# Performance work log

Measured on AMD Instinct MI355X. Metric: run time of the kernel, lower is better.

## Reference

```python
import jax, jax.numpy as jnp
import numpy as np

D, H, KVH, HD, FF = 768, 12, 4, 64, 2048
N_REP = H // KVH
EPS = 1e-6


def rmsnorm(x, w):
    # Faithful to source: norm = ||x|| * n^{-1/2}; eps added to norm (not inside sqrt)
    norm = jnp.sqrt(jnp.sum(x * x, axis=-1, keepdims=True)) * (x.shape[-1] ** -0.5)
    return w * x / (norm + EPS)


def rope_tables(seq_len, head_dim, base=10000.0):
    inv_freq = 1.0 / (base ** (np.arange(0, head_dim, 2, dtype=np.float32) / head_dim))
    t = np.arange(seq_len, dtype=np.float32)
    freqs = np.einsum('i,j->ij', t, inv_freq)  # [S, HD/2]
    emb = np.concatenate([freqs, freqs], axis=-1)  # [S, HD]
    return jnp.asarray(np.cos(emb)), jnp.asarray(np.sin(emb))


def rotate_half(x):
    h = x.shape[-1] // 2
    return jnp.concatenate([-x[..., h:], x[..., :h]], axis=-1)


def setup_inputs() -> dict:
    key = jax.random.key(0)
    ks = jax.random.split(key, 9)
    s = 0.02
    return {
        'x': jax.random.normal(ks[0], (2, 2048, D), jnp.float32),
        'Wq': jax.random.normal(ks[1], (H * HD, D), jnp.float32) * s,
        'Wk': jax.random.normal(ks[2], (KVH * HD, D), jnp.float32) * s,
        'Wv': jax.random.normal(ks[3], (KVH * HD, D), jnp.float32) * s,
        'Wo': jax.random.normal(ks[4], (D, H * HD), jnp.float32) * s,
        'Wgate': jax.random.normal(ks[5], (FF, D), jnp.float32) * s,
        'Wup': jax.random.normal(ks[6], (FF, D), jnp.float32) * s,
        'Wdown': jax.random.normal(ks[7], (D, FF), jnp.float32) * s,
        'g1': jnp.ones((D,), jnp.float32),
        'g2': jnp.ones((D,), jnp.float32),
    }


def reference(x, Wq, Wk, Wv, Wo, Wgate, Wup, Wdown, g1, g2):
    B, S, _ = x.shape
    # ---- attention sublayer (pre-norm) ----
    xn = rmsnorm(x, g1)
    q = (xn @ Wq.T).reshape(B, S, H, HD).transpose(0, 2, 1, 3)      # [B,H,S,HD]
    k = (xn @ Wk.T).reshape(B, S, KVH, HD).transpose(0, 2, 1, 3)    # [B,KVH,S,HD]
    v = (xn @ Wv.T).reshape(B, S, KVH, HD).transpose(0, 2, 1, 3)
    cos, sin = rope_tables(S, HD)                                   # [S,HD]
    q = q * cos + rotate_half(q) * sin
    k = k * cos + rotate_half(k) * sin
    # repeat kv heads to match q heads
    k = jnp.repeat(k, N_REP, axis=1)                                # [B,H,S,HD]
    v = jnp.repeat(v, N_REP, axis=1)
    scores = jnp.einsum('bhqd,bhkd->bhqk', q, k) / jnp.sqrt(jnp.float32(HD))
    causal = jnp.tril(jnp.ones((S, S), bool))
    scores = jnp.where(causal, scores, jnp.finfo(scores.dtype).min)
    attn = jax.nn.softmax(scores, axis=-1)
    out = jnp.einsum('bhqk,bhkd->bhqd', attn, v)                    # [B,H,S,HD]
    out = out.transpose(0, 2, 1, 3).reshape(B, S, H * HD) @ Wo.T
    x = x + out
    # ---- SwiGLU FFN sublayer (pre-norm) ----
    xn2 = rmsnorm(x, g2)
    ff = (jax.nn.silu(xn2 @ Wgate.T) * (xn2 @ Wup.T)) @ Wdown.T
    return x + ff
```

## Files before the change

### kernel.cpp

```cpp
#include <hip/hip_runtime.h>
#include <hip/hip_bf16.h>
#include <math.h>

typedef __bf16 bf16;
typedef __attribute__((ext_vector_type(8))) __bf16 bf16x8;
typedef __attribute__((ext_vector_type(4))) __bf16 bf16x4;
typedef __attribute__((ext_vector_type(4))) float f32x4;

#define MFMA16(a,b,c) __builtin_amdgcn_mfma_f32_16x16x32_bf16(a,b,c,0,0,0)

#define BATCH 2
#define SEQ   2048
#define DMODEL 768
#define NH    12
#define NKV   4
#define NREP  3
#define HD    64
#define FFDIM 2048
#define ROWS  (BATCH*SEQ)

#define QSCALE 0.18033688011112042f
#define LOG2E  1.4426950408889634f

#define WB(N) asm volatile("s_waitcnt vmcnt(" #N ")\n\ts_barrier" ::: "memory")
#define BAR() asm volatile("s_barrier" ::: "memory")

__device__ __forceinline__ void gl2lds16(const bf16* g, bf16* l) {
  __builtin_amdgcn_global_load_lds(
      (const __attribute__((address_space(1))) void*)g,
      (__attribute__((address_space(3))) void*)l, 16, 0, 0);
}

struct Cvt7 { const float* s[7]; bf16* d[7]; int n[7]; };
__global__ __launch_bounds__(256) void cvt_all_kernel(Cvt7 c) {
  int seg = blockIdx.y;
  const float* __restrict__ src = c.s[seg];
  bf16* __restrict__ dst = c.d[seg];
  int n = c.n[seg];
  int stride = gridDim.x * 256;
  for (int i = blockIdx.x * 256 + threadIdx.x; i < n; i += stride)
    dst[i] = (bf16)src[i];
}

__global__ __launch_bounds__(256) void rope_tab_kernel(float* __restrict__ tab) {
  int id = blockIdx.x * 256 + threadIdx.x;
  int j = id >> 11, s = id & 2047;
  float inv = expf(-(float)j * (9.210340371976184f / 32.0f));
  float ang = (float)s * inv;
  tab[id] = cosf(ang);
  tab[65536 + id] = sinf(ang);
}

__global__ __launch_bounds__(192) void rmsnorm_kernel(const float* __restrict__ x,
    const float* __restrict__ g, bf16* __restrict__ out) {
  int row = blockIdx.x;
  const float* xr = x + (size_t)row * DMODEL;
  int t = threadIdx.x;
  f32x4 v = *(const f32x4*)(xr + t * 4);
  float ss = v[0] * v[0] + v[1] * v[1] + v[2] * v[2] + v[3] * v[3];
  #pragma unroll
  for (int off = 32; off; off >>= 1) ss += __shfl_xor(ss, off, 64);
  __shared__ float red[3];
  if ((t & 63) == 0) red[t >> 6] = ss;
  __syncthreads();
  float total = red[0] + red[1] + red[2];
  float norm = sqrtf(total) * 0.03608439182435161f;
  float sc = 1.0f / (norm + 1e-6f);
  f32x4 gv = *(const f32x4*)(g + t * 4);
  bf16x4 o;
  #pragma unroll
  for (int i = 0; i < 4; ++i) o[i] = (bf16)(gv[i] * v[i] * sc);
  *(bf16x4*)(out + (size_t)row * DMODEL + t * 4) = o;
}

__global__ __launch_bounds__(512, 6) void gemm_out_kernel(const bf16* __restrict__ A,
    const bf16* __restrict__ B, float* __restrict__ C, const float* __restrict__ R,
    int N, int K) {
  __shared__ __align__(16) bf16 At[2][3][64 * 32];
  __shared__ __align__(16) bf16 Bt[2][3][64 * 32];
  int t = threadIdx.x;
  int g = t >> 8;
  int tt = t & 255;
  int lane = t & 63;
  int w = (t >> 6) & 3;
  int l15 = lane & 15, lq = lane >> 4;
  int wrow = (w >> 1) * 32, wcol = (w & 1) * 32;

  int flat = blockIdx.y * 12 + blockIdx.x;
  int f2 = (flat & 7) * 96 + (flat >> 3);
  int col0 = (f2 % 12) * 64, row0 = (f2 / 12) * 64;

  const int KH = K >> 1;
  const int NS = KH / 32;
  const bf16* Ag = A + (size_t)(row0 + (tt >> 2)) * K + g * KH + (tt & 3) * 8;
  const bf16* Bg = B + (size_t)(col0 + (tt >> 2)) * K + g * KH + (tt & 3) * 8;

  #pragma unroll
  for (int s = 0; s < 3; ++s) {
    gl2lds16(Ag + s * 32, At[g][s] + tt * 8);
    gl2lds16(Bg + s * 32, Bt[g][s] + tt * 8);
  }

  f32x4 zero = {0.f, 0.f, 0.f, 0.f};
  f32x4 acc[2][2];
  #pragma unroll
  for (int m = 0; m < 2; ++m)
    #pragma unroll
    for (int n = 0; n < 2; ++n) acc[m][n] = zero;

  #define OG_COMPUTE(slot) do {                                              \
    const bf16* at = At[g][slot]; const bf16* bt = Bt[g][slot];              \
    bf16x8 af[2], bb[2];                                                     \
    _Pragma("unroll")                                                        \
    for (int m = 0; m < 2; ++m)                                              \
      af[m] = *(const bf16x8*)(at + (wrow + m * 16 + l15) * 32 + lq * 8);    \
    _Pragma("unroll")                                                        \
    for (int n = 0; n < 2; ++n)                                              \
      bb[n] = *(const bf16x8*)(bt + (wcol + n * 16 + l15) * 32 + lq * 8);    \
    _Pragma("unroll")                                                        \
    for (int m = 0; m < 2; ++m)                                              \
      _Pragma("unroll")                                                      \
      for (int n = 0; n < 2; ++n)                                            \
        acc[m][n] = MFMA16(af[m], bb[n], acc[m][n]);                         \
  } while (0)

  int slot = 0;
  for (int k = 0; k < NS - 2; ++k) {
    WB(4);
    OG_COMPUTE(slot);
    BAR();
    if (k <= NS - 4) {
      int ks = (k + 3) * 32;
      gl2lds16(Ag + ks, At[g][slot] + tt * 8);
      gl2lds16(Bg + ks, Bt[g][slot] + tt * 8);
    }
    slot = (slot == 2) ? 0 : slot + 1;
  }
  for (int k = NS - 2; k < NS; ++k) {
    WB(0);
    OG_COMPUTE(slot);
    slot = (slot == 2) ? 0 : slot + 1;
  }
  #undef OG_COMPUTE

  __syncthreads();
  float* Cl = (float*)&At[0][0][0];
  if (g == 1) {
    #pragma unroll
    for (int m = 0; m < 2; ++m)
      #pragma unroll
      for (int n = 0; n < 2; ++n)
        #pragma unroll
        for (int r = 0; r < 4; ++r)
          Cl[(wrow + m * 16 + lq * 4 + r) * 64 + wcol + n * 16 + l15] = acc[m][n][r];
  }
  __syncthreads();
  if (g == 0) {
    #pragma unroll
    for (int m = 0; m < 2; ++m)
      #pragma unroll
      for (int n = 0; n < 2; ++n)
        #pragma unroll
        for (int r = 0; r < 4; ++r) {
          int row = wrow + m * 16 + lq * 4 + r;
          int col = wcol + n * 16 + l15;
          size_t idx = (size_t)(row0 + row) * N + col0 + col;
          C[idx] = acc[m][n][r] + Cl[row * 64 + col] + R[idx];
        }
  }
}

__global__ __launch_bounds__(256) void gemm_qkv_kernel(const bf16* __restrict__ A,
    const bf16* __restrict__ Wcat, const float* __restrict__ tab,
    bf16* __restrict__ Qh, bf16* __restrict__ Kh, bf16* __restrict__ Vt) {
  __shared__ __align__(16) bf16 At[4][64 * 32];
  __shared__ __align__(16) bf16 Bt[4][128 * 32];
  const int K = DMODEL;
  int t = threadIdx.x, lane = t & 63, wave = t >> 6;
  int l15 = lane & 15, lq = lane >> 4;
  int wrow = (wave >> 1) * 32, wcol = (wave & 1) * 64;
  int row0 = blockIdx.y * 64, col0 = blockIdx.x * 128;
  const bf16* Ag  = A + (size_t)(row0 + (t >> 2)) * K + (t & 3) * 8;
  const bf16* Bg0 = Wcat + (size_t)(col0 + (t >> 2)) * K + (t & 3) * 8;
  const bf16* Bg1 = Bg0 + (size_t)64 * K;
  const int NS = K / 32;

  #pragma unroll
  for (int s = 0; s < 4; ++s) {
    int ks = s * 32;
    gl2lds16(Ag + ks,  At[s] + t * 8);
    gl2lds16(Bg0 + ks, Bt[s] + t * 8);
    gl2lds16(Bg1 + ks, Bt[s] + 2048 + t * 8);
  }

  f32x4 zero = {0.f, 0.f, 0.f, 0.f};
  f32x4 acc[2][4];
  #pragma unroll
  for (int m = 0; m < 2; ++m)
    #pragma unroll
    for (int n = 0; n < 4; ++n) acc[m][n] = zero;

  #define QK_COMPUTE(slot) do {                                              \
    const bf16* at = At[slot]; const bf16* bt = Bt[slot];                    \
    bf16x8 af[2], bfr[4];                                                    \
    _Pragma("unroll")                                                        \
    for (int m = 0; m < 2; ++m)                                              \
      af[m] = *(const bf16x8*)(at + (wrow + m * 16 + l15) * 32 + lq * 8);    \
    _Pragma("unroll")                                                        \
    for (int n = 0; n < 4; ++n)                                              \
      bfr[n] = *(const bf16x8*)(bt + (wcol + n * 16 + l15) * 32 + lq * 8);   \
    _Pragma("unroll")                                                        \
    for (int m = 0; m < 2; ++m)                                              \
      _Pragma("unroll")                                                      \
      for (int n = 0; n < 4; ++n)                                            \
        acc[m][n] = MFMA16(af[m], bfr[n], acc[m][n]);                        \
  } while (0)

  for (int k = 0; k < NS - 3; ++k) {
    WB(9);
    QK_COMPUTE(k & 3);
    BAR();
    if (k <= NS - 5) {
      int ks = (k + 4) * 32;
      gl2lds16(Ag + ks,  At[k & 3] + t * 8);
      gl2lds16(Bg0 + ks, Bt[k & 3] + t * 8);
      gl2lds16(Bg1 + ks, Bt[k & 3] + 2048 + t * 8);
    }
  }
  for (int k = NS - 3; k < NS; ++k) {
    WB(0);
    QK_COMPUTE(k & 3);
  }
  #undef QK_COMPUTE

  int b = row0 >> 11;
  int s0 = (row0 & 2047) + wrow + lq * 4;
  int colw = col0 + wcol;
  if (colw < 768) {
    int h = colw >> 6;
    f32x4 cv[2][2], sv[2][2];
    #pragma unroll
    for (int m = 0; m < 2; ++m)
      #pragma unroll
      for (int jh = 0; jh < 2; ++jh) {
        const float* cp = tab + (jh * 16 + l15) * 2048 + s0 + m * 16;
        cv[m][jh] = *(const f32x4*)cp;
        sv[m][jh] = *(const f32x4*)(cp + 65536);
      }
    #pragma unroll
    for (int m = 0; m < 2; ++m)
      #pragma unroll
      for (int n = 0; n < 4; ++n) {
        float sgn = (n < 2) ? -1.f : 1.f;
        #pragma unroll
        for (int r = 0; r < 4; ++r) {
          float c = cv[m][n & 1][r], si = sv[m][n & 1][r];
          float rp = (acc[m][n][r] * c + sgn * acc[m][n ^ 2][r] * si) * QSCALE;
          Qh[((size_t)(b * NH + h) * SEQ + s0 + m * 16 + r) * 64 + n * 16 + l15] = (bf16)rp;
        }
      }
  } else if (colw < 1024) {
    int kh = (colw - 768) >> 6;
    f32x4 cv[2][2], sv[2][2];
    #pragma unroll
    for (int m = 0; m < 2; ++m)
      #pragma unroll
      for (int jh = 0; jh < 2; ++jh) {
        const float* cp = tab + (jh * 16 + l15) * 2048 + s0 + m * 16;
        cv[m][jh] = *(const f32x4*)cp;
        sv[m][jh] = *(const f32x4*)(cp + 65536);
      }
    #pragma unroll
    for (int m = 0; m < 2; ++m)
      #pragma unroll
      for (int n = 0; n < 4; ++n) {
        float sgn = (n < 2) ? -1.f : 1.f;
        #pragma unroll
        for (int r = 0; r < 4; ++r) {
          float c = cv[m][n & 1][r], si = sv[m][n & 1][r];
          float rp = acc[m][n][r] * c + sgn * acc[m][n ^ 2][r] * si;
          Kh[((size_t)(b * NKV + kh) * SEQ + s0 + m * 16 + r) * 64 + n * 16 + l15] = (bf16)rp;
        }
      }
  } else {
    int vh = (colw - 1024) >> 6;
    #pragma unroll
    for (int m = 0; m < 2; ++m)
      #pragma unroll
      for (int n = 0; n < 4; ++n) {
        bf16x4 pv;
        #pragma unroll
        for (int r = 0; r < 4; ++r) pv[r] = (bf16)acc[m][n][r];
        *(bf16x4*)(Vt + ((size_t)(b * NKV + vh) * 64 + n * 16 + l15) * SEQ + s0 + m * 16) = pv;
      }
  }
}

__global__ __launch_bounds__(512, 4) void gemm_gu_kernel(const bf16* __restrict__ A,
    const bf16* __restrict__ Wg, const bf16* __restrict__ Wu, bf16* __restrict__ H) {
  __shared__ __align__(16) bf16 At[3][128 * 32];
  __shared__ __align__(16) bf16 Bgt[3][128 * 32];
  __shared__ __align__(16) bf16 But[3][128 * 32];
  const int K = DMODEL;
  int t = threadIdx.x, lane = t & 63, wave = t >> 6;
  int l15 = lane & 15, lq = lane >> 4;
  int wrow = (wave >> 2) * 64, wcol = (wave & 3) * 32;
  int row0 = blockIdx.y * 128, col0 = blockIdx.x * 128;
  const bf16* Ag = A  + (size_t)(row0 + (t >> 2)) * K + (t & 3) * 8;
  const bf16* Gg = Wg + (size_t)(col0 + (t >> 2)) * K + (t & 3) * 8;
  const bf16* Ug = Wu + (size_t)(col0 + (t >> 2)) * K + (t & 3) * 8;
  const int NS = K / 32;

  #pragma unroll
  for (int s = 0; s < 3; ++s) {
    int ks = s * 32;
    gl2lds16(Ag + ks, At[s] + t * 8);
    gl2lds16(Gg + ks, Bgt[s] + t * 8);
    gl2lds16(Ug + ks, But[s] + t * 8);
  }

  f32x4 zero = {0.f, 0.f, 0.f, 0.f};
  f32x4 ag[4][2], au[4][2];
  #pragma unroll
  for (int m = 0; m < 4; ++m)
    #pragma unroll
    for (int n = 0; n < 2; ++n) { ag[m][n] = zero; au[m][n] = zero; }

  #define GU_COMPUTE(slot) do {                                              \
    const bf16* at = At[slot];                                               \
    const bf16* bgt = Bgt[slot]; const bf16* but = But[slot];                \
    bf16x8 af[4], bg[2], bu[2];                                              \
    _Pragma("unroll")                                                        \
    for (int m = 0; m < 4; ++m)                                              \
      af[m] = *(const bf16x8*)(at + (wrow + m * 16 + l15) * 32 + lq * 8);    \
    _Pragma("unroll")                                                        \
    for (int n = 0; n < 2; ++n) {                                            \
      bg[n] = *(const bf16x8*)(bgt + (wcol + n * 16 + l15) * 32 + lq * 8);   \
      bu[n] = *(const bf16x8*)(but + (wcol + n * 16 + l15) * 32 + lq * 8);   \
    }                                                                        \
    _Pragma("unroll")                                                        \
    for (int m = 0; m < 4; ++m)                                              \
      _Pragma("unroll")                                                      \
      for (int n = 0; n < 2; ++n) {                                          \
        ag[m][n] = MFMA16(af[m], bg[n], ag[m][n]);                           \
        au[m][n] = MFMA16(af[m], bu[n], au[m][n]);                           \
      }                                                                      \
  } while (0)

  int slot = 0;
  for (int k = 0; k < NS - 2; ++k) {
    WB(6);
    GU_COMPUTE(slot);
    BAR();
    if (k <= NS - 4) {
      int ks = (k + 3) * 32;
      gl2lds16(Ag + ks, At[slot] + t * 8);
      gl2lds16(Gg + ks, Bgt[slot] + t * 8);
      gl2lds16(Ug + ks, But[slot] + t * 8);
    }
    slot = (slot == 2) ? 0 : slot + 1;
  }
  for (int k = NS - 2; k < NS; ++k) {
    WB(0);
    GU_COMPUTE(slot);
    slot = (slot == 2) ? 0 : slot + 1;
  }
  #undef GU_COMPUTE

  #pragma unroll
  for (int m = 0; m < 4; ++m)
    #pragma unroll
    for (int n = 0; n < 2; ++n)
      #pragma unroll
      for (int r = 0; r < 4; ++r) {
        int row = row0 + wrow + m * 16 + lq * 4 + r;
        int col = col0 + wcol + n * 16 + l15;
        float g = ag[m][n][r], u = au[m][n][r];
        float sg = g / (1.f + __builtin_amdgcn_exp2f(-g * LOG2E));
        H[(size_t)row * FFDIM + col] = (bf16)(sg * u);
      }
}

__global__ __launch_bounds__(256) void attn_kernel(const bf16* __restrict__ Qh,
    const bf16* __restrict__ Kh, const bf16* __restrict__ Vt, bf16* __restrict__ out) {
  __shared__ __align__(16) bf16 Kl0[2][64 * 32];
  __shared__ __align__(16) bf16 Kl1[2][64 * 32];
  __shared__ __align__(16) bf16 Vl0[2][64 * 32];
  __shared__ __align__(16) bf16 Vl1[2][64 * 32];
  __shared__ __align__(16) bf16 P[4][16 * 80];

  int idx = blockIdx.x;
  int qt = 31 - (idx / 24);
  int bh = idx % 24;
  int q0blk = qt * 64;
  int b = bh / NH, h = bh % NH;
  int kvh = h / NREP;
  int t = threadIdx.x;
  int lane = t & 63, wave = t >> 6;
  int l15 = lane & 15, lq = lane >> 4;
  int qw = q0blk + wave * 16;
  const bf16* Qb = Qh + (size_t)(b * NH + h) * SEQ * 64;
  const bf16* Kb = Kh + (size_t)(b * NKV + kvh) * SEQ * 64;
  const bf16* Vb = Vt + (size_t)(b * NKV + kvh) * 64 * SEQ;

  bf16x8 bq0 = *(const bf16x8*)(Qb + (size_t)(qw + l15) * 64 + lq * 8);
  bf16x8 bq1 = *(const bf16x8*)(Qb + (size_t)(qw + l15) * 64 + 32 + lq * 8);

  const bf16* Kg = Kb + (size_t)(t >> 2) * 64 + (t & 3) * 8;
  const bf16* Vg = Vb + (size_t)(t >> 2) * SEQ + (t & 3) * 8;
  bf16* Pw = P[wave];
  int Pwq = l15 * 80, lq8 = lq * 8, lq4 = lq * 4;
  const int NS = qt + 1;

  #pragma unroll
  for (int s = 0; s < 2; ++s) {
    int ks = (s < NS ? s : NS - 1) * 64;
    gl2lds16(Kg + (size_t)ks * 64,      Kl0[s] + t * 8);
    gl2lds16(Kg + (size_t)ks * 64 + 32, Kl1[s] + t * 8);
    gl2lds16(Vg + ks,                   Vl0[s] + t * 8);
    gl2lds16(Vg + ks + 32,              Vl1[s] + t * 8);
  }

  f32x4 zero = {0.f, 0.f, 0.f, 0.f};
  f32x4 o[4];
  o[0] = zero; o[1] = zero; o[2] = zero; o[3] = zero;
  float l_r = 0.f;

  #define ATTN_STEP(kk, slot) do {                                           \
    int k0 = (kk) * 64;                                                      \
    const bf16* kl0 = Kl0[slot]; const bf16* kl1 = Kl1[slot];                \
    const bf16* vl0 = Vl0[slot]; const bf16* vl1 = Vl1[slot];                \
    f32x4 s[4];                                                              \
    _Pragma("unroll")                                                        \
    for (int c = 0; c < 4; ++c) {                                            \
      bf16x8 ak0 = *(const bf16x8*)(kl0 + (c * 16 + l15) * 32 + lq8);        \
      bf16x8 ak1 = *(const bf16x8*)(kl1 + (c * 16 + l15) * 32 + lq8);        \
      s[c] = zero;                                                           \
      s[c] = MFMA16(ak0, bq0, s[c]);                                         \
      s[c] = MFMA16(ak1, bq1, s[c]);                                         \
    }                                                                        \
    if (k0 + 63 > qw) {                                                      \
      int qmk = qw + l15 - k0 - lq4;                                         \
      _Pragma("unroll")                                                      \
      for (int c = 0; c < 4; ++c)                                            \
        _Pragma("unroll")                                                    \
        for (int r = 0; r < 4; ++r)                                          \
          if (c * 16 + r > qmk) s[c][r] = -INFINITY;                         \
    }                                                                        \
    _Pragma("unroll")                                                        \
    for (int c = 0; c < 4; ++c) {                                            \
      bf16x4 pe;                                                             \
      _Pragma("unroll")                                                      \
      for (int r = 0; r < 4; ++r) {                                          \
        float e = __builtin_amdgcn_exp2f(s[c][r]);                           \
        l_r += e;                                                            \
        pe[r] = (bf16)e;                                                     \
      }                                                                      \
      *(bf16x4*)(Pw + Pwq + c * 16 + lq4) = pe;                              \
    }                                                                        \
    bf16x8 bp0 = *(const bf16x8*)(Pw + Pwq + lq8);                           \
    bf16x8 bp1 = *(const bf16x8*)(Pw + Pwq + 32 + lq8);                      \
    _Pragma("unroll")                                                        \
    for (int n = 0; n < 4; ++n) {                                            \
      bf16x8 av0 = *(const bf16x8*)(vl0 + (n * 16 + l15) * 32 + lq8);        \
      bf16x8 av1 = *(const bf16x8*)(vl1 + (n * 16 + l15) * 32 + lq8);        \
      o[n] = MFMA16(av0, bp0, o[n]);                                         \
      o[n] = MFMA16(av1, bp1, o[n]);                                         \
    }                                                                        \
  } while (0)

  for (int k = 0; k < NS - 1; ++k) {
    WB(4);
    ATTN_STEP(k, k & 1);
    BAR();
    if (k <= NS - 3) {
      int ks = (k + 2) * 64;
      gl2lds16(Kg + (size_t)ks * 64,      Kl0[k & 1] + t * 8);
      gl2lds16(Kg + (size_t)ks * 64 + 32, Kl1[k & 1] + t * 8);
      gl2lds16(Vg + ks,                   Vl0[k & 1] + t * 8);
      gl2lds16(Vg + ks + 32,              Vl1[k & 1] + t * 8);
    }
  }
  {
    WB(0);
    ATTN_STEP(NS - 1, (NS - 1) & 1);
  }
  #undef ATTN_STEP

  float lt = l_r;
  lt += __shfl_xor(lt, 16, 64);
  lt += __shfl_xor(lt, 32, 64);
  float inv = 1.f / lt;
  int q = qw + l15;
  bf16* orow = out + (size_t)(b * SEQ + q) * DMODEL + h * 64;
  #pragma unroll
  for (int n = 0; n < 4; ++n) {
    bf16x4 po;
    #pragma unroll
    for (int r = 0; r < 4; ++r) po[r] = (bf16)(o[n][r] * inv);
    *(bf16x4*)(orow + n * 16 + lq4) = po;
  }
}

extern "C" void kernel_launch(void* const* d_in, const int* in_sizes, int n_in,
                              void* d_out, int out_size, void* d_ws, size_t ws_size,
                              hipStream_t stream) {
  const float* x     = (const float*)d_in[0];
  const float* Wq    = (const float*)d_in[1];
  const float* Wk    = (const float*)d_in[2];
  const float* Wv    = (const float*)d_in[3];
  const float* Wo    = (const float*)d_in[4];
  const float* Wgate = (const float*)d_in[5];
  const float* Wup   = (const float*)d_in[6];
  const float* Wdown = (const float*)d_in[7];
  const float* g1    = (const float*)d_in[8];
  const float* g2    = (const float*)d_in[9];
  float* out = (float*)d_out;

  char* ws = (char*)d_ws;
  size_t off = 0;
  auto alloc = [&](size_t bytes) { size_t o = off; off += (bytes + 255) & ~(size_t)255; return o; };
  size_t o_tab  = alloc((size_t)2 * 32 * 2048 * 4);
  size_t o_x1   = alloc((size_t)4096 * 768 * 4);
  size_t o_xn   = alloc((size_t)4096 * 768 * 2);
  size_t o_Qh   = alloc((size_t)2 * 12 * 2048 * 64 * 2);
  size_t o_Kh   = alloc((size_t)2 * 4 * 2048 * 64 * 2);
  size_t o_Vt   = alloc((size_t)2 * 4 * 64 * 2048 * 2);
  size_t o_ao   = alloc((size_t)4096 * 768 * 2);
  size_t o_H    = alloc((size_t)4096 * 2048 * 2);
  size_t o_Wcat = alloc((size_t)1280 * 768 * 2);
  size_t o_Wo   = alloc((size_t)768 * 768 * 2);
  size_t o_Wgu  = alloc((size_t)4096 * 768 * 2);
  size_t o_Wdn  = alloc((size_t)768 * 2048 * 2);
  if (ws_size < off) return;

  float* tab  = (float*)(ws + o_tab);
  float* fx1  = (float*)(ws + o_x1);
  bf16* bxn   = (bf16*)(ws + o_xn);
  bf16* bQh   = (bf16*)(ws + o_Qh);
  bf16* bKh   = (bf16*)(ws + o_Kh);
  bf16* bVt   = (bf16*)(ws + o_Vt);
  bf16* bao   = (bf16*)(ws + o_ao);
  bf16* bH    = (bf16*)(ws + o_H);
  bf16* bWcat = (bf16*)(ws + o_Wcat);
  bf16* bWo   = (bf16*)(ws + o_Wo);
  bf16* bWgu  = (bf16*)(ws + o_Wgu);
  bf16* bWdn  = (bf16*)(ws + o_Wdn);

  rope_tab_kernel<<<256, 256, 0, stream>>>(tab);

  Cvt7 c;
  c.s[0] = Wq;    c.d[0] = bWcat;              c.n[0] = 768 * 768;
  c.s[1] = Wk;    c.d[1] = bWcat + 768 * 768;  c.n[1] = 256 * 768;
  c.s[2] = Wv;    c.d[2] = bWcat + 1024 * 768; c.n[2] = 256 * 768;
  c.s[3] = Wo;    c.d[3] = bWo;                c.n[3] = 768 * 768;
  c.s[4] = Wgate; c.d[4] = bWgu;               c.n[4] = 2048 * 768;
  c.s[5] = Wup;   c.d[5] = bWgu + 2048 * 768;  c.n[5] = 2048 * 768;
  c.s[6] = Wdown; c.d[6] = bWdn;               c.n[6] = 768 * 2048;
  cvt_all_kernel<<<dim3(256, 7), 256, 0, stream>>>(c);

  rmsnorm_kernel<<<4096, 192, 0, stream>>>(x, g1, bxn);
  gemm_qkv_kernel<<<dim3(10, 64), 256, 0, stream>>>(bxn, bWcat, tab, bQh, bKh, bVt);
  attn_kernel<<<dim3(768), 256, 0, stream>>>(bQh, bKh, bVt, bao);
  gemm_out_kernel<<<dim3(12, 64), 512, 0, stream>>>(bao, bWo, fx1, x, 768, 768);

  rmsnorm_kernel<<<4096, 192, 0, stream>>>(fx1, g2, bxn);
  gemm_gu_kernel<<<dim3(16, 32), 512, 0, stream>>>(bxn, bWgu, bWgu + 2048 * 768, bH);
  gemm_out_kernel<<<dim3(12, 64), 512, 0, stream>>>(bH, bWdn, out, fx1, 768, 2048);
}
```

Baseline: 246.5 us.

## Fold rope table into convert kernel; use 4-wave gate/up GEMM with 64x64 wave tiles

The rope cos/sin table generation moves into the weight-conversion launch as an extra grid segment, which removes one kernel launch. The gate/up GEMM drops from 8 to 4 waves per block. Each wave now computes a 64x64 tile for both gate and up, reusing its A fragments across more MFMAs and loading the gate and up B fragments in turn. Each thread issues twice as many async global-to-LDS loads, and the per-wave accumulator count doubles, which raises register pressure and may cut occupancy and latency hiding.

```diff
diff --git a/kernel.cpp b/kernel.cpp
--- a/kernel.cpp
+++ b/kernel.cpp
@@ -31,24 +31,24 @@
       (__attribute__((address_space(3))) void*)l, 16, 0, 0);
 }
 
-struct Cvt7 { const float* s[7]; bf16* d[7]; int n[7]; };
+struct Cvt7 { const float* s[7]; bf16* d[7]; int n[7]; float* tab; };
 __global__ __launch_bounds__(256) void cvt_all_kernel(Cvt7 c) {
   int seg = blockIdx.y;
+  if (seg == 7) {
+    int id = blockIdx.x * 256 + threadIdx.x;
+    int j = id >> 11, s = id & 2047;
+    float inv = expf(-(float)j * (9.210340371976184f / 32.0f));
+    float ang = (float)s * inv;
+    c.tab[id] = cosf(ang);
+    c.tab[65536 + id] = sinf(ang);
+    return;
+  }
   const float* __restrict__ src = c.s[seg];
   bf16* __restrict__ dst = c.d[seg];
   int n = c.n[seg];
   int stride = gridDim.x * 256;
   for (int i = blockIdx.x * 256 + threadIdx.x; i < n; i += stride)
     dst[i] = (bf16)src[i];
-}
-
-__global__ __launch_bounds__(256) void rope_tab_kernel(float* __restrict__ tab) {
-  int id = blockIdx.x * 256 + threadIdx.x;
-  int j = id >> 11, s = id & 2047;
-  float inv = expf(-(float)j * (9.210340371976184f / 32.0f));
-  float ang = (float)s * inv;
-  tab[id] = cosf(ang);
-  tab[65536 + id] = sinf(ang);
 }
 
 __global__ __launch_bounds__(192) void rmsnorm_kernel(const float* __restrict__ x,
@@ -296,7 +296,7 @@
   }
 }
 
-__global__ __launch_bounds__(512, 4) void gemm_gu_kernel(const bf16* __restrict__ A,
+__global__ __launch_bounds__(256, 2) void gemm_gu_kernel(const bf16* __restrict__ A,
     const bf16* __restrict__ Wg, const bf16* __restrict__ Wu, bf16* __restrict__ H) {
   __shared__ __align__(16) bf16 At[3][128 * 32];
   __shared__ __align__(16) bf16 Bgt[3][128 * 32];
@@ -304,59 +304,72 @@
   const int K = DMODEL;
   int t = threadIdx.x, lane = t & 63, wave = t >> 6;
   int l15 = lane & 15, lq = lane >> 4;
-  int wrow = (wave >> 2) * 64, wcol = (wave & 3) * 32;
+  int wrow = (wave >> 1) * 64, wcol = (wave & 1) * 64;
   int row0 = blockIdx.y * 128, col0 = blockIdx.x * 128;
-  const bf16* Ag = A  + (size_t)(row0 + (t >> 2)) * K + (t & 3) * 8;
-  const bf16* Gg = Wg + (size_t)(col0 + (t >> 2)) * K + (t & 3) * 8;
-  const bf16* Ug = Wu + (size_t)(col0 + (t >> 2)) * K + (t & 3) * 8;
+  const bf16* Ag0 = A  + (size_t)(row0 + (t >> 2)) * K + (t & 3) * 8;
+  const bf16* Ag1 = Ag0 + (size_t)64 * K;
+  const bf16* Gg0 = Wg + (size_t)(col0 + (t >> 2)) * K + (t & 3) * 8;
+  const bf16* Gg1 = Gg0 + (size_t)64 * K;
+  const bf16* Ug0 = Wu + (size_t)(col0 + (t >> 2)) * K + (t & 3) * 8;
+  const bf16* Ug1 = Ug0 + (size_t)64 * K;
   const int NS = K / 32;
 
   #pragma unroll
   for (int s = 0; s < 3; ++s) {
     int ks = s * 32;
-    gl2lds16(Ag + ks, At[s] + t * 8);
-    gl2lds16(Gg + ks, Bgt[s] + t * 8);
-    gl2lds16(Ug + ks, But[s] + t * 8);
+    gl2lds16(Ag0 + ks, At[s] + t * 8);
+    gl2lds16(Ag1 + ks, At[s] + 2048 + t * 8);
+    gl2lds16(Gg0 + ks, Bgt[s] + t * 8);
+    gl2lds16(Gg1 + ks, Bgt[s] + 2048 + t * 8);
+    gl2lds16(Ug0 + ks, But[s] + t * 8);
+    gl2lds16(Ug1 + ks, But[s] + 2048 + t * 8);
   }
 
   f32x4 zero = {0.f, 0.f, 0.f, 0.f};
-  f32x4 ag[4][2], au[4][2];
+  f32x4 ag[4][4], au[4][4];
   #pragma unroll
   for (int m = 0; m < 4; ++m)
     #pragma unroll
-    for (int n = 0; n < 2; ++n) { ag[m][n] = zero; au[m][n] = zero; }
+    for (int n = 0; n < 4; ++n) { ag[m][n] = zero; au[m][n] = zero; }
 
   #define GU_COMPUTE(slot) do {                                              \
     const bf16* at = At[slot];                                               \
     const bf16* bgt = Bgt[slot]; const bf16* but = But[slot];                \
-    bf16x8 af[4], bg[2], bu[2];                                              \
+    bf16x8 af[4], bb[4];                                                     \
     _Pragma("unroll")                                                        \
     for (int m = 0; m < 4; ++m)                                              \
       af[m] = *(const bf16x8*)(at + (wrow + m * 16 + l15) * 32 + lq * 8);    \
     _Pragma("unroll")                                                        \
-    for (int n = 0; n < 2; ++n) {                                            \
-      bg[n] = *(const bf16x8*)(bgt + (wcol + n * 16 + l15) * 32 + lq * 8);   \
-      bu[n] = *(const bf16x8*)(but + (wcol + n * 16 + l15) * 32 + lq * 8);   \
-    }                                                                        \
+    for (int n = 0; n < 4; ++n)                                              \
+      bb[n] = *(const bf16x8*)(bgt + (wcol + n * 16 + l15) * 32 + lq * 8);   \
     _Pragma("unroll")                                                        \
     for (int m = 0; m < 4; ++m)                                              \
       _Pragma("unroll")                                                      \
-      for (int n = 0; n < 2; ++n) {                                          \
-        ag[m][n] = MFMA16(af[m], bg[n], ag[m][n]);                           \
-        au[m][n] = MFMA16(af[m], bu[n], au[m][n]);                           \
-      }                                                                      \
+      for (int n = 0; n < 4; ++n)                                            \
+        ag[m][n] = MFMA16(af[m], bb[n], ag[m][n]);                           \
+    _Pragma("unroll")                                                        \
+    for (int n = 0; n < 4; ++n)                                              \
+      bb[n] = *(const bf16x8*)(but + (wcol + n * 16 + l15) * 32 + lq * 8);   \
+    _Pragma("unroll")                                                        \
+    for (int m = 0; m < 4; ++m)                                              \
+      _Pragma("unroll")                                                      \
+      for (int n = 0; n < 4; ++n)                                            \
+        au[m][n] = MFMA16(af[m], bb[n], au[m][n]);                           \
   } while (0)
 
   int slot = 0;
   for (int k = 0; k < NS - 2; ++k) {
-    WB(6);
+    WB(12);
     GU_COMPUTE(slot);
     BAR();
     if (k <= NS - 4) {
       int ks = (k + 3) * 32;
-      gl2lds16(Ag + ks, At[slot] + t * 8);
-      gl2lds16(Gg + ks, Bgt[slot] + t * 8);
-      gl2lds16(Ug + ks, But[slot] + t * 8);
+      gl2lds16(Ag0 + ks, At[slot] + t * 8);
+      gl2lds16(Ag1 + ks, At[slot] + 2048 + t * 8);
+      gl2lds16(Gg0 + ks, Bgt[slot] + t * 8);
+      gl2lds16(Gg1 + ks, Bgt[slot] + 2048 + t * 8);
+      gl2lds16(Ug0 + ks, But[slot] + t * 8);
+      gl2lds16(Ug1 + ks, But[slot] + 2048 + t * 8);
     }
     slot = (slot == 2) ? 0 : slot + 1;
   }
@@ -370,7 +383,7 @@
   #pragma unroll
   for (int m = 0; m < 4; ++m)
     #pragma unroll
-    for (int n = 0; n < 2; ++n)
+    for (int n = 0; n < 4; ++n)
       #pragma unroll
       for (int r = 0; r < 4; ++r) {
         int row = row0 + wrow + m * 16 + lq * 4 + r;
@@ -547,8 +560,6 @@
   bf16* bWgu  = (bf16*)(ws + o_Wgu);
   bf16* bWdn  = (bf16*)(ws + o_Wdn);
 
-  rope_tab_kernel<<<256, 256, 0, stream>>>(tab);
-
   Cvt7 c;
   c.s[0] = Wq;    c.d[0] = bWcat;              c.n[0] = 768 * 768;
   c.s[1] = Wk;    c.d[1] = bWcat + 768 * 768;  c.n[1] = 256 * 768;
@@ -557,7 +568,8 @@
   c.s[4] = Wgate; c.d[4] = bWgu;               c.n[4] = 2048 * 768;
   c.s[5] = Wup;   c.d[5] = bWgu + 2048 * 768;  c.n[5] = 2048 * 768;
   c.s[6] = Wdown; c.d[6] = bWdn;               c.n[6] = 768 * 2048;
-  cvt_all_kernel<<<dim3(256, 7), 256, 0, stream>>>(c);
+  c.tab = tab;
+  cvt_all_kernel<<<dim3(256, 8), 256, 0, stream>>>(c);
 
   rmsnorm_kernel<<<4096, 192, 0, stream>>>(x, g1, bxn);
   gemm_qkv_kernel<<<dim3(10, 64), 256, 0, stream>>>(bxn, bWcat, tab, bQh, bKh, bVt);
@@ -565,6 +577,6 @@
   gemm_out_kernel<<<dim3(12, 64), 512, 0, stream>>>(bao, bWo, fx1, x, 768, 768);
 
   rmsnorm_kernel<<<4096, 192, 0, stream>>>(fx1, g2, bxn);
-  gemm_gu_kernel<<<dim3(16, 32), 512, 0, stream>>>(bxn, bWgu, bWgu + 2048 * 768, bH);
+  gemm_gu_kernel<<<dim3(16, 32), 256, 0, stream>>>(bxn, bWgu, bWgu + 2048 * 768, bH);
   gemm_out_kernel<<<dim3(12, 64), 512, 0, stream>>>(bH, bWdn, out, fx1, 768, 2048);
 }
```

Result: no change. 242.4 us (-1.6%).
